# Optimization experiments

Hardware: AMD Instinct MI355X
Metric: run time of the kernel (lower is better)

Reference implementation:

```python
import jax, jax.numpy as jnp
import numpy as np

B, N, D, E, H = 4, 2048, 512, 16, 1024
CAP = max(4, min(N, int(N * 2.0 / E)))   # eval capacity_factor = 2.0 -> 256
EPS = 1e-9
THRESH = 0.2  # second_threshold_eval


def setup_inputs() -> dict:
    key = jax.random.key(0)
    ks = jax.random.split(key, 10)
    f32 = jnp.float32
    return {
        "X": jax.random.normal(ks[0], (B, N, D), f32),
        "probs": jax.random.uniform(ks[1], (B, N), f32),
        "W1": jax.random.normal(ks[2], (D, D), f32) * (1.0 / np.sqrt(D)),
        "b1": jnp.zeros((D,), f32),
        "Wg": jax.random.normal(ks[3], (D, E), f32),  # Top2Gating uses randn init
        "We1": jax.random.normal(ks[4], (E, D, H), f32) * (1.0 / np.sqrt(D)),
        "We2": jax.random.normal(ks[5], (E, H, D), f32) * (1.0 / np.sqrt(H)),
        "W3": jax.random.normal(ks[6], (D, 4), f32) * (1.0 / np.sqrt(D)),
        "b3": jnp.zeros((4,), f32),
        "W4": jax.random.normal(ks[7], (4, 1), f32) * 0.5,
        "b4": jnp.zeros((1,), f32),
    }


def top2_gating(x, Wg, probs):
    # x: [B, N, D] -> raw gates [B, N, E]
    raw = jax.nn.softmax(jnp.einsum('bnd,de->bne', x, Wg), axis=-1)
    dt = raw.dtype

    gate1 = jnp.max(raw, axis=-1)
    idx1 = jnp.argmax(raw, axis=-1)
    mask1 = jax.nn.one_hot(idx1, E, dtype=dt)
    density_proxy = raw

    raw_wo1 = raw * (1.0 - mask1)
    gate2 = jnp.max(raw_wo1, axis=-1)
    idx2 = jnp.argmax(raw_wo1, axis=-1)
    mask2 = jax.nn.one_hot(idx2, E, dtype=dt)

    denom = gate1 + gate2 + EPS
    gate1 = gate1 / denom
    gate2 = gate2 / denom

    # load-balancing loss (computed but wrapper discards it)
    density1 = jnp.mean(mask1, axis=-2)
    loss = jnp.mean(jnp.mean(density_proxy, axis=-2) * density1) * float(E ** 2)

    # second policy == 'random'
    mask2 = mask2 * (probs < (gate2 / max(THRESH, EPS))).astype(dt)[..., None]

    # exclusive cumsum along the group dim gives position within each expert
    pos1 = (jnp.cumsum(mask1, axis=-2) - mask1) * mask1          # [B, N, E]
    mask1 = mask1 * (pos1 < float(CAP)).astype(dt)
    mask1_count = jnp.sum(mask1, axis=-2, keepdims=True)
    mask1_flat = jnp.sum(mask1, axis=-1)                          # [B, N]
    pos1_flat = jnp.sum(pos1, axis=-1)
    gate1 = gate1 * mask1_flat

    pos2 = ((jnp.cumsum(mask2, axis=-2) - mask2) + mask1_count) * mask2
    mask2 = mask2 * (pos2 < float(CAP)).astype(dt)
    mask2_flat = jnp.sum(mask2, axis=-1)
    pos2_flat = jnp.sum(pos2, axis=-1)
    gate2 = gate2 * mask2_flat

    # safe one-hot: out-of-range positions map to all-zeros (jax.nn.one_hot semantics)
    oh_p1 = jax.nn.one_hot(pos1_flat.astype(jnp.int32), CAP, dtype=dt)
    oh_p2 = jax.nn.one_hot(pos2_flat.astype(jnp.int32), CAP, dtype=dt)
    oh_e1 = jax.nn.one_hot(idx1, E, dtype=dt)
    oh_e2 = jax.nn.one_hot(idx2, E, dtype=dt)

    combine = ((gate1 * mask1_flat)[..., None, None] * oh_e1[..., :, None] * oh_p1[..., None, :]
               + (gate2 * mask2_flat)[..., None, None] * oh_e2[..., :, None] * oh_p2[..., None, :])
    dispatch = (combine != 0).astype(dt)
    return dispatch, combine, loss


def reference(X, probs, W1, b1, Wg, We1, We2, W3, b3, W4, b4):
    h = X @ W1 + b1                                              # linear1
    dispatch, combine, loss = top2_gating(h, Wg, probs)
    exp_in = jnp.einsum('bnd,bnec->ebcd', h, dispatch)           # dispatch
    hid = jax.nn.leaky_relu(jnp.einsum('ebcd,edh->ebch', exp_in, We1))
    exp_out = jnp.einsum('ebch,ehd->ebcd', hid, We2)             # experts
    moe_out = jnp.einsum('bnec,ebcd->bnd', combine, exp_out)     # combine
    out = (moe_out @ W3 + b3) @ W4 + b4                          # hidden3 -> act3
    return out
```

## Files before the change

### kernel.cpp

```cpp
#include <hip/hip_runtime.h>
#include <hip/hip_bf16.h>

#define NB 4
#define NN 2048
#define ND 512
#define NE 16
#define NH 1024
#define CAP 256
#define NTOK (NB*NN)

typedef __attribute__((ext_vector_type(8))) short bf16x8;
typedef __attribute__((ext_vector_type(4))) float f32x4;
typedef __attribute__((ext_vector_type(8))) unsigned short u16x8;

__device__ __forceinline__ void gload16(const void* gsrc, void* lds) {
    __builtin_amdgcn_global_load_lds((const __attribute__((address_space(1))) void*)gsrc,
                                     (__attribute__((address_space(3))) void*)lds, 16, 0, 0);
}
__device__ __forceinline__ unsigned short f2bf(float f) {
    union { __hip_bfloat16 b; unsigned short u; } v; v.b = __float2bfloat16(f); return v.u;
}

__global__ __launch_bounds__(256) void prep_w_kernel(const float* __restrict__ W1,
                                                     const float* __restrict__ Wg,
                                                     unsigned short* __restrict__ W1B,
                                                     float* __restrict__ WcT,
                                                     float* __restrict__ zbuf) {
    const int tid = threadIdx.x;
    int bid = blockIdx.x;
    if (bid < 128) {
        if (bid == 0) zbuf[tid] = 0.f;
        const int w = tid >> 6, l = tid & 63;
        const int d = bid * 4 + w;
        float a0 = 0.f, a1 = 0.f, a2 = 0.f, a3 = 0.f, a4 = 0.f, a5 = 0.f, a6 = 0.f, a7 = 0.f;
        float a8 = 0.f, a9 = 0.f, aA = 0.f, aB = 0.f, aC = 0.f, aD = 0.f, aE = 0.f, aF = 0.f;
        #pragma unroll
        for (int ch = 0; ch < 8; ++ch) {
            float x = W1[(size_t)d * ND + ch * 64 + l];
            const float4* wg4 = (const float4*)(Wg + (size_t)(ch * 64 + l) * NE);
            float4 g0 = wg4[0], g1 = wg4[1], g2 = wg4[2], g3 = wg4[3];
            a0 = fmaf(x, g0.x, a0); a1 = fmaf(x, g0.y, a1); a2 = fmaf(x, g0.z, a2); a3 = fmaf(x, g0.w, a3);
            a4 = fmaf(x, g1.x, a4); a5 = fmaf(x, g1.y, a5); a6 = fmaf(x, g1.z, a6); a7 = fmaf(x, g1.w, a7);
            a8 = fmaf(x, g2.x, a8); a9 = fmaf(x, g2.y, a9); aA = fmaf(x, g2.z, aA); aB = fmaf(x, g2.w, aB);
            aC = fmaf(x, g3.x, aC); aD = fmaf(x, g3.y, aD); aE = fmaf(x, g3.z, aE); aF = fmaf(x, g3.w, aF);
        }
        float accs[16] = {a0, a1, a2, a3, a4, a5, a6, a7, a8, a9, aA, aB, aC, aD, aE, aF};
        #pragma unroll
        for (int off = 32; off >= 1; off >>= 1)
            #pragma unroll
            for (int e = 0; e < 16; ++e) accs[e] += __shfl_xor(accs[e], off);
        #pragma unroll
        for (int e = 0; e < 16; ++e)
            if (l == e) WcT[e * ND + d] = accs[e];
        return;
    }
    bid -= 128;
    {
        int dblk = bid >> 1, hblk = bid & 1;
        const float* src = W1 + (size_t)(dblk * 64) * ND + hblk * 256 + tid;
        unsigned short* dst = W1B + (size_t)(dblk * 512 + hblk * 256 + tid) * 64;
        float v[64];
        #pragma unroll
        for (int j = 0; j < 64; ++j) v[j] = src[(size_t)j * ND];
        #pragma unroll
        for (int q = 0; q < 8; ++q) {
            u16x8 o;
            #pragma unroll
            for (int j = 0; j < 8; ++j) o[j] = f2bf(v[q * 8 + j]);
            *(u16x8*)(dst + q * 8) = o;
        }
    }
}

__global__ __launch_bounds__(256, 8) void gating_stream_kernel(const float* __restrict__ X,
                                                               const float* __restrict__ WcT,
                                                               const float* __restrict__ probs,
                                                               const float* __restrict__ b3,
                                                               const float* __restrict__ W4,
                                                               const float* __restrict__ b4,
                                                               const float* __restrict__ We1,
                                                               const float* __restrict__ We2,
                                                               const float* __restrict__ W3,
                                                               unsigned short* __restrict__ Xbf,
                                                               unsigned short* __restrict__ We1B,
                                                               float* __restrict__ u,
                                                               int* __restrict__ idx1a, int* __restrict__ idx2a,
                                                               float* __restrict__ g1a, float* __restrict__ g2a,
                                                               float* __restrict__ out) {
    __shared__ float wc[NE * ND];
    const int tid = threadIdx.x;
    int bid = blockIdx.x;
    const int w = tid >> 6, l = tid & 63;
    if (bid < 512) {
        #pragma unroll
        for (int i = 0; i < 32; ++i) wc[tid + 256 * i] = WcT[tid + 256 * i];
        float c0v = b4[0];
        #pragma unroll
        for (int j = 0; j < 4; ++j) c0v += b3[j] * W4[j];
        __syncthreads();
        const float4* wc4 = (const float4*)wc;
        for (int j = 0; j < 4; ++j) {
            int tok = bid * 16 + j * 4 + w;
            const float4* xrow = (const float4*)(X + (size_t)tok * ND);
            float4 x0 = xrow[l], x1 = xrow[l + 64];
            {
                ushort4 o0, o1;
                o0.x = f2bf(x0.x); o0.y = f2bf(x0.y); o0.z = f2bf(x0.z); o0.w = f2bf(x0.w);
                o1.x = f2bf(x1.x); o1.y = f2bf(x1.y); o1.z = f2bf(x1.z); o1.w = f2bf(x1.w);
                *(ushort4*)(Xbf + (size_t)tok * ND + 4 * l) = o0;
                *(ushort4*)(Xbf + (size_t)tok * ND + 256 + 4 * l) = o1;
            }
            float acc[NE];
            #pragma unroll
            for (int e = 0; e < NE; ++e) {
                float4 w0 = wc4[e * 128 + l], w1 = wc4[e * 128 + l + 64];
                acc[e] = x0.x * w0.x + x0.y * w0.y + x0.z * w0.z + x0.w * w0.w
                       + x1.x * w1.x + x1.y * w1.y + x1.z * w1.z + x1.w * w1.w;
            }
            #pragma unroll
            for (int off = 32; off >= 1; off >>= 1)
                #pragma unroll
                for (int e = 0; e < NE; ++e) acc[e] += __shfl_xor(acc[e], off);

            if (l == 0) {
                float m = acc[0];
                #pragma unroll
                for (int e = 1; e < NE; ++e) m = fmaxf(m, acc[e]);
                float s = 0.f;
                #pragma unroll
                for (int e = 0; e < NE; ++e) { acc[e] = expf(acc[e] - m); s += acc[e]; }
                float inv = 1.f / s;
                #pragma unroll
                for (int e = 0; e < NE; ++e) acc[e] *= inv;
                int i1 = 0; float g1 = acc[0];
                #pragma unroll
                for (int e = 1; e < NE; ++e) if (acc[e] > g1) { g1 = acc[e]; i1 = e; }
                int i2 = -1; float g2 = -1.f;
                #pragma unroll
                for (int e = 0; e < NE; ++e) if (e != i1 && acc[e] > g2) { g2 = acc[e]; i2 = e; }
                float denom = g1 + g2 + 1e-9f;
                float g1n = g1 / denom, g2n = g2 / denom;
                bool flag = probs[tok] < (g2n / 0.2f);
                idx1a[tok] = i1;
                idx2a[tok] = flag ? i2 : -1;
                g1a[tok] = g1n;
                g2a[tok] = g2n;
                out[tok] = c0v;
            }
        }
        return;
    }
    const int sb = bid - 512;
    if (sb & 1) {
        const int unit = sb >> 1;
        const int e = unit >> 5, rem = unit & 31;
        const int dblk = rem >> 2, hq = rem & 3;
        const float* src = We1 + (size_t)e * ND * NH + (size_t)(dblk * 64) * NH + hq * 256 + tid;
        unsigned short* dst = We1B + ((size_t)(e * 8 + dblk) * NH + hq * 256 + tid) * 64;
        #pragma unroll
        for (int half = 0; half < 2; ++half) {
            float v[32];
            #pragma unroll
            for (int j = 0; j < 32; ++j) v[j] = src[(size_t)(half * 32 + j) * NH];
            #pragma unroll
            for (int q = 0; q < 4; ++q) {
                u16x8 o;
                #pragma unroll
                for (int j = 0; j < 8; ++j) o[j] = f2bf(v[q * 8 + j]);
                *(u16x8*)(dst + half * 32 + q * 8) = o;
            }
        }
        return;
    }
    {
        const int ub = sb >> 1;
        float* vvs = wc;
        {
            int d = tid * 2;
            float s0 = 0.f, s1 = 0.f;
            #pragma unroll
            for (int j = 0; j < 4; ++j) {
                s0 += W3[d * 4 + j] * W4[j];
                s1 += W3[(d + 1) * 4 + j] * W4[j];
            }
            vvs[d] = s0; vvs[d + 1] = s1;
        }
        __syncthreads();
        const float4* vv4 = (const float4*)vvs;
        const float4 v0 = vv4[l], v1 = vv4[l + 64];
        float sums[8];
        #pragma unroll
        for (int i = 0; i < 8; ++i) {
            int gr = ub * 32 + w * 8 + i;
            const float4* row = (const float4*)(We2 + (size_t)gr * ND);
            float4 a0 = row[l], a1 = row[l + 64];
            sums[i] = a0.x * v0.x + a0.y * v0.y + a0.z * v0.z + a0.w * v0.w
                    + a1.x * v1.x + a1.y * v1.y + a1.z * v1.z + a1.w * v1.w;
        }
        #pragma unroll
        for (int off = 32; off >= 1; off >>= 1)
            #pragma unroll
            for (int i = 0; i < 8; ++i) sums[i] += __shfl_xor(sums[i], off);
        if (l == 0) {
            int gr0 = ub * 32 + w * 8;
            #pragma unroll
            for (int i = 0; i < 8; ++i) u[gr0 + i] = sums[i];
        }
    }
}

__global__ __launch_bounds__(512) void scan_linear1_kernel(const int* __restrict__ idx1a,
                                                           const int* __restrict__ idx2a,
                                                           int* __restrict__ slot_token,
                                                           const unsigned short* __restrict__ Xbf,
                                                           const unsigned short* __restrict__ W1B,
                                                           const float* __restrict__ b1,
                                                           unsigned short* __restrict__ hbf) {
    __shared__ char smem[65536];
    const int tid = threadIdx.x;
    const int w = tid >> 6, l = tid & 63;
    if (blockIdx.x < 64) {
        const int bb = blockIdx.x;
        const int b = bb >> 4, e = bb & 15;
        int* cnt1 = (int*)smem;
        int* cnt2 = cnt1 + 8;
        int* slot = slot_token + (e * NB + b) * CAP;
        const unsigned long long below = (l == 0) ? 0ull : ((1ull << l) - 1ull);
        const int base0 = w * 256;
        int c1 = 0, c2 = 0;
        #pragma unroll
        for (int it = 0; it < 4; ++it) {
            int n = base0 + it * 64 + l;
            c1 += __popcll(__ballot(idx1a[b * NN + n] == e));
            c2 += __popcll(__ballot(idx2a[b * NN + n] == e));
        }
        if (l == 0) { cnt1[w] = c1; cnt2[w] = c2; }
        __syncthreads();
        int b1c = 0, t1 = 0, b2c = 0, t2 = 0;
        #pragma unroll
        for (int i = 0; i < 8; ++i) {
            int v1 = cnt1[i], v2 = cnt2[i];
            if (i < w) { b1c += v1; b2c += v2; }
            t1 += v1; t2 += v2;
        }
        const int start2 = (t1 < CAP) ? t1 : CAP;
        int c = b1c;
        #pragma unroll
        for (int it = 0; it < 4; ++it) {
            int n = base0 + it * 64 + l;
            bool p = (idx1a[b * NN + n] == e);
            unsigned long long m = __ballot(p);
            int pre = __popcll(m & below);
            if (p) { int pos = c + pre; if (pos < CAP) slot[pos] = n; }
            c += __popcll(m);
        }
        c = start2 + b2c;
        #pragma unroll
        for (int it = 0; it < 4; ++it) {
            int n = base0 + it * 64 + l;
            bool p = (idx2a[b * NN + n] == e);
            unsigned long long m = __ballot(p);
            int pre = __popcll(m & below);
            if (p) { int pos = c + pre; if (pos < CAP) slot[pos] = n | (1 << 30); }
            c += __popcll(m);
        }
        int nfill = start2 + t2; nfill = (nfill < CAP) ? nfill : CAP;
        for (int i = nfill + tid; i < CAP; i += 512) slot[i] = -1;
        return;
    }
    const int lb = blockIdx.x - 64;
    const int m0 = (lb >> 2) * 128, n0 = (lb & 3) * 128;
    const int wm = w >> 1, wn = w & 1;
    const int lr = l & 15, lk = l >> 4;
    char* Ash0 = smem;
    char* Bsh0 = smem + 32768;

    auto stage = [&](int Ks, int buf) {
        #pragma unroll
        for (int i = 0; i < 2; ++i) {
            int o = i * 8192 + tid * 16;
            int r = o >> 7, bb = o & 127;
            int sb2 = bb ^ ((r & 7) << 4);
            gload16((const char*)Xbf + ((size_t)(m0 + r) * ND + Ks * 64) * 2 + sb2,
                    Ash0 + buf * 16384 + i * 8192 + w * 1024);
            gload16((const char*)W1B + ((size_t)(Ks * 512 + n0 + r) * 64) * 2 + sb2,
                    Bsh0 + buf * 16384 + i * 8192 + w * 1024);
        }
    };

    f32x4 acc[2][4] = {};
    stage(0, 0);
    __syncthreads();
    for (int Ks = 0; Ks < 8; ++Ks) {
        int buf = Ks & 1;
        if (Ks < 7) stage(Ks + 1, buf ^ 1);
        #pragma unroll
        for (int k32 = 0; k32 < 2; ++k32) {
            int kb = (k32 * 32 + 8 * lk) * 2;
            bf16x8 a[2], bfr[4];
            #pragma unroll
            for (int mi = 0; mi < 2; ++mi) {
                int row = wm * 32 + mi * 16 + lr;
                a[mi] = *(const bf16x8*)(Ash0 + buf * 16384 + row * 128 + (kb ^ ((row & 7) << 4)));
            }
            #pragma unroll
            for (int ni = 0; ni < 4; ++ni) {
                int row = wn * 64 + ni * 16 + lr;
                bfr[ni] = *(const bf16x8*)(Bsh0 + buf * 16384 + row * 128 + (kb ^ ((row & 7) << 4)));
            }
            #pragma unroll
            for (int mi = 0; mi < 2; ++mi)
                #pragma unroll
                for (int ni = 0; ni < 4; ++ni)
                    acc[mi][ni] = __builtin_amdgcn_mfma_f32_16x16x32_bf16(a[mi], bfr[ni], acc[mi][ni], 0, 0, 0);
        }
        __syncthreads();
    }
    #pragma unroll
    for (int mi = 0; mi < 2; ++mi)
        #pragma unroll
        for (int ni = 0; ni < 4; ++ni) {
            int col = n0 + wn * 64 + ni * 16 + lr;
            float bb1 = b1[col];
            #pragma unroll
            for (int r = 0; r < 4; ++r) {
                int m = m0 + wm * 32 + mi * 16 + lk * 4 + r;
                hbf[(size_t)m * ND + col] = f2bf(acc[mi][ni][r] + bb1);
            }
        }
}

__global__ __launch_bounds__(512) void expert_mfma_kernel(const unsigned short* __restrict__ hbf,
                                                          const unsigned short* __restrict__ We1B,
                                                          const float* __restrict__ u,
                                                          const int* __restrict__ slot_token,
                                                          const float* __restrict__ zbuf,
                                                          const float* __restrict__ g1a,
                                                          const float* __restrict__ g2a,
                                                          float* __restrict__ out) {
    __shared__ char Ash[65536];
    __shared__ char Bsh[2][32768];
    __shared__ float u_lds[NH];
    __shared__ float sbuf[8][64];
    __shared__ int toks[64];
    const int tid = threadIdx.x;
    const int w = tid >> 6, l = tid & 63;
    const int lr = l & 15, lk = l >> 4;
    const int bid = blockIdx.x;
    const int e = (bid & 7) | ((bid >> 7) << 3);
    const int chunk = (bid >> 3) & 15;
    const int b = chunk >> 2, c0 = (chunk & 3) * 64;

    if (tid < 64) toks[tid] = slot_token[(e * NB + b) * CAP + c0 + tid];
    u_lds[tid] = u[e * NH + tid];
    u_lds[tid + 512] = u[e * NH + tid + 512];
    __syncthreads();
    #pragma unroll
    for (int i = 0; i < 8; ++i) {
        int r = i * 8 + w;
        int t = toks[r];
        int tok = t & 2047;
        int sb = (l * 16) ^ ((r & 7) << 4);
        const char* src = (t >= 0) ? ((const char*)hbf + ((size_t)(b * NN + tok) * ND) * 2 + sb)
                                   : ((const char*)zbuf + sb);
        gload16(src, Ash + i * 8192 + w * 1024);
    }
    auto stageB = [&](int s, int buf) {
        int Hc = s >> 4, Ks = s & 15;
        const size_t base = ((size_t)(e * 8 + (Ks >> 1)) * NH + Hc * 512) * 64 + (Ks & 1) * 32;
        #pragma unroll
        for (int i = 0; i < 4; ++i) {
            int r = i * 128 + w * 16 + (l >> 2);
            int swzr = ((r >> 1) & 3) << 4;
            int ebyte = ((l & 3) * 16) ^ swzr;
            gload16((const char*)We1B + (base + (size_t)r * 64) * 2 + ebyte,
                    Bsh[buf] + i * 8192 + w * 1024);
        }
    };
    f32x4 acc[4][4] = {};
    float srow[4][4] = {};
    stageB(0, 0);
    __syncthreads();
    for (int s = 0; s < 32; ++s) {
        int buf = s & 1;
        if (s < 31) stageB(s + 1, buf ^ 1);
        int Ks = s & 15;
        bf16x8 a[4], bb[4];
        #pragma unroll
        for (int mi = 0; mi < 4; ++mi) {
            int row = mi * 16 + lr;
            int kb = (Ks * 64 + lk * 16) ^ ((row & 7) << 4);
            a[mi] = *(const bf16x8*)(Ash + row * 1024 + kb);
        }
        #pragma unroll
        for (int ni = 0; ni < 4; ++ni) {
            int row = w * 64 + ni * 16 + lr;
            int kb = (lk * 16) ^ (((row >> 1) & 3) << 4);
            bb[ni] = *(const bf16x8*)(Bsh[buf] + row * 64 + kb);
        }
        #pragma unroll
        for (int mi = 0; mi < 4; ++mi)
            #pragma unroll
            for (int ni = 0; ni < 4; ++ni)
                acc[mi][ni] = __builtin_amdgcn_mfma_f32_16x16x32_bf16(a[mi], bb[ni], acc[mi][ni], 0, 0, 0);
        if ((s & 15) == 15) {
            int Hc = s >> 4;
            #pragma unroll
            for (int ni = 0; ni < 4; ++ni) {
                float uu = u_lds[Hc * 512 + w * 64 + ni * 16 + lr];
                #pragma unroll
                for (int mi = 0; mi < 4; ++mi)
                    #pragma unroll
                    for (int r = 0; r < 4; ++r) {
                        float x = acc[mi][ni][r];
                        x = (x > 0.f) ? x : 0.01f * x;
                        srow[mi][r] = fmaf(x, uu, srow[mi][r]);
                        acc[mi][ni][r] = 0.f;
                    }
            }
        }
        __syncthreads();
    }
    #pragma unroll
    for (int off = 1; off < 16; off <<= 1)
        #pragma unroll
        for (int mi = 0; mi < 4; ++mi)
            #pragma unroll
            for (int r = 0; r < 4; ++r)
                srow[mi][r] += __shfl_xor(srow[mi][r], off);
    if (lr == 0) {
        #pragma unroll
        for (int mi = 0; mi < 4; ++mi)
            #pragma unroll
            for (int r = 0; r < 4; ++r)
                sbuf[w][mi * 16 + lk * 4 + r] = srow[mi][r];
    }
    __syncthreads();
    if (tid < 64) {
        float s = 0.f;
        #pragma unroll
        for (int q = 0; q < 8; ++q) s += sbuf[q][tid];
        int v = toks[tid];
        if (v >= 0) {
            int tok = v & 2047;
            float g = (v & (1 << 30)) ? g2a[b * NN + tok] : g1a[b * NN + tok];
            atomicAdd(out + b * NN + tok, s * g);
        }
    }
}

extern "C" void kernel_launch(void* const* d_in, const int* in_sizes, int n_in,
                              void* d_out, int out_size, void* d_ws, size_t ws_size,
                              hipStream_t stream) {
    const float* X    = (const float*)d_in[0];
    const float* probs= (const float*)d_in[1];
    const float* W1   = (const float*)d_in[2];
    const float* b1   = (const float*)d_in[3];
    const float* Wg   = (const float*)d_in[4];
    const float* We1  = (const float*)d_in[5];
    const float* We2  = (const float*)d_in[6];
    const float* W3   = (const float*)d_in[7];
    const float* b3   = (const float*)d_in[8];
    const float* W4   = (const float*)d_in[9];
    const float* b4   = (const float*)d_in[10];
    float* out = (float*)d_out;

    char* ws = (char*)d_ws;
    size_t off = 0;
    auto alloc = [&](size_t bytes) { void* p = ws + off; off += (bytes + 255) & ~(size_t)255; return p; };
    unsigned short* Xbf  = (unsigned short*)alloc((size_t)NTOK * ND * 2);
    unsigned short* hbf  = (unsigned short*)alloc((size_t)NTOK * ND * 2);
    unsigned short* W1B  = (unsigned short*)alloc((size_t)ND * ND * 2);
    unsigned short* We1B = (unsigned short*)alloc((size_t)NE * NH * ND * 2);
    float* WcT     = (float*)alloc(NE * ND * 4);
    float* u       = (float*)alloc(NE * NH * 4);
    float* zbuf    = (float*)alloc(1024);
    int*   idx1a   = (int*)alloc(NTOK * 4);
    int*   idx2a   = (int*)alloc(NTOK * 4);
    float* g1a     = (float*)alloc(NTOK * 4);
    float* g2a     = (float*)alloc(NTOK * 4);
    int*   slot_tok= (int*)alloc(NE * NB * CAP * 4);
    (void)ws_size; (void)in_sizes; (void)n_in; (void)out_size;

    prep_w_kernel<<<144, 256, 0, stream>>>(W1, Wg, W1B, WcT, zbuf);
    gating_stream_kernel<<<1536, 256, 0, stream>>>(X, WcT, probs, b3, W4, b4,
                                                   We1, We2, W3,
                                                   Xbf, We1B, u,
                                                   idx1a, idx2a, g1a, g2a, out);
    scan_linear1_kernel<<<320, 512, 0, stream>>>(idx1a, idx2a, slot_tok,
                                                 Xbf, W1B, b1, hbf);
    expert_mfma_kernel<<<256, 512, 0, stream>>>(hbf, We1B, u, slot_tok, zbuf, g1a, g2a, out);
}
```

Baseline: 79.98 us.

## Move We2·(W3W4) reduction from gating kernel into scan/linear1 kernel

Relocates the 512 blocks computing u = We2·(W3·W4) out of the gating/stream kernel into 64 extra blocks of the scan/linear1 kernel, each handling 256 rows over four passes. It also drops the (256,8) launch-bound occupancy hint on the gating kernel. The aim is to rebalance work between kernels so the bandwidth-heavy We2 read overlaps with the linear1 MFMA and scan blocks instead of competing with the We1 conversion traffic. The scan kernel's blocks run with 512 threads, so W3·W4 is now computed one element per thread.

```diff
diff --git a/kernel.cpp b/kernel.cpp
--- a/kernel.cpp
+++ b/kernel.cpp
@@ -72,21 +72,18 @@
     }
 }
 
-__global__ __launch_bounds__(256, 8) void gating_stream_kernel(const float* __restrict__ X,
-                                                               const float* __restrict__ WcT,
-                                                               const float* __restrict__ probs,
-                                                               const float* __restrict__ b3,
-                                                               const float* __restrict__ W4,
-                                                               const float* __restrict__ b4,
-                                                               const float* __restrict__ We1,
-                                                               const float* __restrict__ We2,
-                                                               const float* __restrict__ W3,
-                                                               unsigned short* __restrict__ Xbf,
-                                                               unsigned short* __restrict__ We1B,
-                                                               float* __restrict__ u,
-                                                               int* __restrict__ idx1a, int* __restrict__ idx2a,
-                                                               float* __restrict__ g1a, float* __restrict__ g2a,
-                                                               float* __restrict__ out) {
+__global__ __launch_bounds__(256) void gating_stream_kernel(const float* __restrict__ X,
+                                                            const float* __restrict__ WcT,
+                                                            const float* __restrict__ probs,
+                                                            const float* __restrict__ b3,
+                                                            const float* __restrict__ W4,
+                                                            const float* __restrict__ b4,
+                                                            const float* __restrict__ We1,
+                                                            unsigned short* __restrict__ Xbf,
+                                                            unsigned short* __restrict__ We1B,
+                                                            int* __restrict__ idx1a, int* __restrict__ idx2a,
+                                                            float* __restrict__ g1a, float* __restrict__ g2a,
+                                                            float* __restrict__ out) {
     __shared__ float wc[NE * ND];
     const int tid = threadIdx.x;
     int bid = blockIdx.x;
@@ -150,9 +147,8 @@
         }
         return;
     }
-    const int sb = bid - 512;
-    if (sb & 1) {
-        const int unit = sb >> 1;
+    {
+        const int unit = bid - 512;
         const int e = unit >> 5, rem = unit & 31;
         const int dblk = rem >> 2, hq = rem & 3;
         const float* src = We1 + (size_t)e * ND * NH + (size_t)(dblk * 64) * NH + hq * 256 + tid;
@@ -169,42 +165,6 @@
                 for (int j = 0; j < 8; ++j) o[j] = f2bf(v[q * 8 + j]);
                 *(u16x8*)(dst + half * 32 + q * 8) = o;
             }
-        }
-        return;
-    }
-    {
-        const int ub = sb >> 1;
-        float* vvs = wc;
-        {
-            int d = tid * 2;
-            float s0 = 0.f, s1 = 0.f;
-            #pragma unroll
-            for (int j = 0; j < 4; ++j) {
-                s0 += W3[d * 4 + j] * W4[j];
-                s1 += W3[(d + 1) * 4 + j] * W4[j];
-            }
-            vvs[d] = s0; vvs[d + 1] = s1;
-        }
-        __syncthreads();
-        const float4* vv4 = (const float4*)vvs;
-        const float4 v0 = vv4[l], v1 = vv4[l + 64];
-        float sums[8];
-        #pragma unroll
-        for (int i = 0; i < 8; ++i) {
-            int gr = ub * 32 + w * 8 + i;
-            const float4* row = (const float4*)(We2 + (size_t)gr * ND);
-            float4 a0 = row[l], a1 = row[l + 64];
-            sums[i] = a0.x * v0.x + a0.y * v0.y + a0.z * v0.z + a0.w * v0.w
-                    + a1.x * v1.x + a1.y * v1.y + a1.z * v1.z + a1.w * v1.w;
-        }
-        #pragma unroll
-        for (int off = 32; off >= 1; off >>= 1)
-            #pragma unroll
-            for (int i = 0; i < 8; ++i) sums[i] += __shfl_xor(sums[i], off);
-        if (l == 0) {
-            int gr0 = ub * 32 + w * 8;
-            #pragma unroll
-            for (int i = 0; i < 8; ++i) u[gr0 + i] = sums[i];
         }
     }
 }
@@ -215,7 +175,11 @@
                                                            const unsigned short* __restrict__ Xbf,
                                                            const unsigned short* __restrict__ W1B,
                                                            const float* __restrict__ b1,
-                                                           unsigned short* __restrict__ hbf) {
+                                                           unsigned short* __restrict__ hbf,
+                                                           const float* __restrict__ We2,
+                                                           const float* __restrict__ W3,
+                                                           const float* __restrict__ W4,
+                                                           float* __restrict__ u) {
     __shared__ char smem[65536];
     const int tid = threadIdx.x;
     const int w = tid >> 6, l = tid & 63;
@@ -268,66 +232,103 @@
         for (int i = nfill + tid; i < CAP; i += 512) slot[i] = -1;
         return;
     }
-    const int lb = blockIdx.x - 64;
-    const int m0 = (lb >> 2) * 128, n0 = (lb & 3) * 128;
-    const int wm = w >> 1, wn = w & 1;
-    const int lr = l & 15, lk = l >> 4;
-    char* Ash0 = smem;
-    char* Bsh0 = smem + 32768;
-
-    auto stage = [&](int Ks, int buf) {
-        #pragma unroll
-        for (int i = 0; i < 2; ++i) {
-            int o = i * 8192 + tid * 16;
-            int r = o >> 7, bb = o & 127;
-            int sb2 = bb ^ ((r & 7) << 4);
-            gload16((const char*)Xbf + ((size_t)(m0 + r) * ND + Ks * 64) * 2 + sb2,
-                    Ash0 + buf * 16384 + i * 8192 + w * 1024);
-            gload16((const char*)W1B + ((size_t)(Ks * 512 + n0 + r) * 64) * 2 + sb2,
-                    Bsh0 + buf * 16384 + i * 8192 + w * 1024);
-        }
-    };
-
-    f32x4 acc[2][4] = {};
-    stage(0, 0);
-    __syncthreads();
-    for (int Ks = 0; Ks < 8; ++Ks) {
-        int buf = Ks & 1;
-        if (Ks < 7) stage(Ks + 1, buf ^ 1);
-        #pragma unroll
-        for (int k32 = 0; k32 < 2; ++k32) {
-            int kb = (k32 * 32 + 8 * lk) * 2;
-            bf16x8 a[2], bfr[4];
-            #pragma unroll
-            for (int mi = 0; mi < 2; ++mi) {
-                int row = wm * 32 + mi * 16 + lr;
-                a[mi] = *(const bf16x8*)(Ash0 + buf * 16384 + row * 128 + (kb ^ ((row & 7) << 4)));
-            }
+    if (blockIdx.x < 320) {
+        const int lb = blockIdx.x - 64;
+        const int m0 = (lb >> 2) * 128, n0 = (lb & 3) * 128;
+        const int wm = w >> 1, wn = w & 1;
+        const int lr = l & 15, lk = l >> 4;
+        char* Ash0 = smem;
+        char* Bsh0 = smem + 32768;
+
+        auto stage = [&](int Ks, int buf) {
+            #pragma unroll
+            for (int i = 0; i < 2; ++i) {
+                int o = i * 8192 + tid * 16;
+                int r = o >> 7, bb = o & 127;
+                int sb2 = bb ^ ((r & 7) << 4);
+                gload16((const char*)Xbf + ((size_t)(m0 + r) * ND + Ks * 64) * 2 + sb2,
+                        Ash0 + buf * 16384 + i * 8192 + w * 1024);
+                gload16((const char*)W1B + ((size_t)(Ks * 512 + n0 + r) * 64) * 2 + sb2,
+                        Bsh0 + buf * 16384 + i * 8192 + w * 1024);
+            }
+        };
+
+        f32x4 acc[2][4] = {};
+        stage(0, 0);
+        __syncthreads();
+        for (int Ks = 0; Ks < 8; ++Ks) {
+            int buf = Ks & 1;
+            if (Ks < 7) stage(Ks + 1, buf ^ 1);
+            #pragma unroll
+            for (int k32 = 0; k32 < 2; ++k32) {
+                int kb = (k32 * 32 + 8 * lk) * 2;
+                bf16x8 a[2], bfr[4];
+                #pragma unroll
+                for (int mi = 0; mi < 2; ++mi) {
+                    int row = wm * 32 + mi * 16 + lr;
+                    a[mi] = *(const bf16x8*)(Ash0 + buf * 16384 + row * 128 + (kb ^ ((row & 7) << 4)));
+                }
+                #pragma unroll
+                for (int ni = 0; ni < 4; ++ni) {
+                    int row = wn * 64 + ni * 16 + lr;
+                    bfr[ni] = *(const bf16x8*)(Bsh0 + buf * 16384 + row * 128 + (kb ^ ((row & 7) << 4)));
+                }
+                #pragma unroll
+                for (int mi = 0; mi < 2; ++mi)
+                    #pragma unroll
+                    for (int ni = 0; ni < 4; ++ni)
+                        acc[mi][ni] = __builtin_amdgcn_mfma_f32_16x16x32_bf16(a[mi], bfr[ni], acc[mi][ni], 0, 0, 0);
+            }
+            __syncthreads();
+        }
+        #pragma unroll
+        for (int mi = 0; mi < 2; ++mi)
             #pragma unroll
             for (int ni = 0; ni < 4; ++ni) {
-                int row = wn * 64 + ni * 16 + lr;
-                bfr[ni] = *(const bf16x8*)(Bsh0 + buf * 16384 + row * 128 + (kb ^ ((row & 7) << 4)));
-            }
-            #pragma unroll
-            for (int mi = 0; mi < 2; ++mi)
-                #pragma unroll
-                for (int ni = 0; ni < 4; ++ni)
-                    acc[mi][ni] = __builtin_amdgcn_mfma_f32_16x16x32_bf16(a[mi], bfr[ni], acc[mi][ni], 0, 0, 0);
+                int col = n0 + wn * 64 + ni * 16 + lr;
+                float bb1 = b1[col];
+                #pragma unroll
+                for (int r = 0; r < 4; ++r) {
+                    int m = m0 + wm * 32 + mi * 16 + lk * 4 + r;
+                    hbf[(size_t)m * ND + col] = f2bf(acc[mi][ni][r] + bb1);
+                }
+            }
+        return;
+    }
+    {
+        const int ub = blockIdx.x - 320;
+        float* vvs = (float*)smem;
+        {
+            float s0 = 0.f;
+            #pragma unroll
+            for (int j = 0; j < 4; ++j) s0 += W3[tid * 4 + j] * W4[j];
+            vvs[tid] = s0;
         }
         __syncthreads();
-    }
-    #pragma unroll
-    for (int mi = 0; mi < 2; ++mi)
-        #pragma unroll
-        for (int ni = 0; ni < 4; ++ni) {
-            int col = n0 + wn * 64 + ni * 16 + lr;
-            float bb1 = b1[col];
-            #pragma unroll
-            for (int r = 0; r < 4; ++r) {
-                int m = m0 + wm * 32 + mi * 16 + lk * 4 + r;
-                hbf[(size_t)m * ND + col] = f2bf(acc[mi][ni][r] + bb1);
-            }
-        }
+        const float4* vv4 = (const float4*)vvs;
+        const float4 v0 = vv4[l], v1 = vv4[l + 64];
+        #pragma unroll
+        for (int pass = 0; pass < 4; ++pass) {
+            float sums[8];
+            #pragma unroll
+            for (int i = 0; i < 8; ++i) {
+                int gr = ub * 256 + pass * 64 + w * 8 + i;
+                const float4* row = (const float4*)(We2 + (size_t)gr * ND);
+                float4 a0 = row[l], a1 = row[l + 64];
+                sums[i] = a0.x * v0.x + a0.y * v0.y + a0.z * v0.z + a0.w * v0.w
+                        + a1.x * v1.x + a1.y * v1.y + a1.z * v1.z + a1.w * v1.w;
+            }
+            #pragma unroll
+            for (int off = 32; off >= 1; off >>= 1)
+                #pragma unroll
+                for (int i = 0; i < 8; ++i) sums[i] += __shfl_xor(sums[i], off);
+            if (l == 0) {
+                int gr0 = ub * 256 + pass * 64 + w * 8;
+                #pragma unroll
+                for (int i = 0; i < 8; ++i) u[gr0 + i] = sums[i];
+            }
+        }
+    }
 }
 
 __global__ __launch_bounds__(512) void expert_mfma_kernel(const unsigned short* __restrict__ hbf,
@@ -483,11 +484,11 @@
     (void)ws_size; (void)in_sizes; (void)n_in; (void)out_size;
 
     prep_w_kernel<<<144, 256, 0, stream>>>(W1, Wg, W1B, WcT, zbuf);
-    gating_stream_kernel<<<1536, 256, 0, stream>>>(X, WcT, probs, b3, W4, b4,
-                                                   We1, We2, W3,
-                                                   Xbf, We1B, u,
+    gating_stream_kernel<<<1024, 256, 0, stream>>>(X, WcT, probs, b3, W4, b4,
+                                                   We1, Xbf, We1B,
                                                    idx1a, idx2a, g1a, g2a, out);
-    scan_linear1_kernel<<<320, 512, 0, stream>>>(idx1a, idx2a, slot_tok,
-                                                 Xbf, W1B, b1, hbf);
+    scan_linear1_kernel<<<384, 512, 0, stream>>>(idx1a, idx2a, slot_tok,
+                                                 Xbf, W1B, b1, hbf,
+                                                 We2, W3, W4, u);
     expert_mfma_kernel<<<256, 512, 0, stream>>>(hbf, We1B, u, slot_tok, zbuf, g1a, g2a, out);
 }
```

Measured after the change: 80.78 us. About the same (+1.0%).
